# Kernel optimization log

Measured on AMD Instinct MI355X. Metric: run time of the kernel, lower is better.

## Reference

```python
import jax, jax.numpy as jnp
import numpy as np

B, N, C_IN, C_INTER = 32, 2048, 512, 512


def setup_inputs() -> dict:
    key = jax.random.key(0)
    ks = jax.random.split(key, 10)
    s_in = 1.0 / np.sqrt(C_IN)
    s_int = 1.0 / np.sqrt(C_INTER)
    return {
        "query": jax.random.normal(ks[0], (B, N, C_IN), jnp.float32),
        "key": jax.random.normal(ks[1], (B, N, C_IN), jnp.float32),
        "Wq": jax.random.normal(ks[2], (C_IN, C_INTER), jnp.float32) * s_in,
        "bq": jnp.zeros((C_INTER,), jnp.float32),
        "Wk": jax.random.normal(ks[3], (C_IN, C_INTER), jnp.float32) * s_in,
        "bk": jnp.zeros((C_INTER,), jnp.float32),
        "Wv": jax.random.normal(ks[4], (C_IN, C_INTER), jnp.float32) * s_in,
        "bv": jnp.zeros((C_INTER,), jnp.float32),
        "Wo": jax.random.normal(ks[5], (C_INTER, C_INTER), jnp.float32) * s_int,
        "bo": jnp.zeros((C_INTER,), jnp.float32),
    }


def reference(query, key, Wq, bq, Wk, bk, Wv, bv, Wo, bo):
    value = key  # value defaults to key in original forward
    q = jnp.einsum("bnc,cd->bnd", query, Wq) + bq   # [B,N,D]
    k = jnp.einsum("bnc,cd->bnd", key, Wk) + bk
    v = jnp.einsum("bnc,cd->bnd", value, Wv) + bv
    d = q.shape[-1]
    # non-standard scaling: divide by d (not sqrt(d))
    scores = jnp.einsum("bqd,bkd->bqk", q, k) / d    # [B,N,N]
    attn = jax.nn.softmax(scores, axis=-1)
    n_kv = attn.shape[-1]
    # second non-standard scaling: divide by number of keys
    out = jnp.einsum("bqk,bkd->bqd", attn, v) / n_kv
    return jnp.einsum("bnd,de->bne", out, Wo) + bo
```

## Files before the change

### kernel.cpp

```cpp
#include <hip/hip_runtime.h>
#include <stdint.h>

typedef unsigned short u16;
typedef __attribute__((ext_vector_type(8))) short bf16x8;
typedef __attribute__((ext_vector_type(4))) float f32x4;
typedef __attribute__((ext_vector_type(2))) unsigned int u32x2;
typedef __attribute__((ext_vector_type(4))) unsigned int u32x4;

__device__ __forceinline__ float bf2f(u16 u) {
  union { unsigned int i; float f; } v; v.i = ((unsigned int)u) << 16; return v.f;
}
__device__ __forceinline__ u16 f2bf(float f) {
  union { float f; unsigned int i; } v; v.f = f;
  unsigned int x = v.i;
  return (u16)((x + 0x7fffu + ((x >> 16) & 1u)) >> 16);
}

__device__ __forceinline__ void async16(const void* g, void* l) {
  __builtin_amdgcn_global_load_lds(
      (const __attribute__((address_space(1))) void*)g,
      (__attribute__((address_space(3))) void*)l, 16, 0, 0);
}

__global__ __launch_bounds__(256) void cast_f32_to_bf16(
    const float* __restrict__ x, u16* __restrict__ y, long n) {
  long i = ((long)blockIdx.x * blockDim.x + threadIdx.x) * 8;
  long stride = (long)gridDim.x * blockDim.x * 8;
  for (long j = i; j < n; j += stride) {
    float4 a = ((const float4*)(x + j))[0];
    float4 b = ((const float4*)(x + j))[1];
    u32x4 o;
    o.x = (unsigned)f2bf(a.x) | ((unsigned)f2bf(a.y) << 16);
    o.y = (unsigned)f2bf(a.z) | ((unsigned)f2bf(a.w) << 16);
    o.z = (unsigned)f2bf(b.x) | ((unsigned)f2bf(b.y) << 16);
    o.w = (unsigned)f2bf(b.z) | ((unsigned)f2bf(b.w) << 16);
    __builtin_nontemporal_store(o, (u32x4*)(y + j));
  }
}

__global__ __launch_bounds__(256) void castKT(
    const float* __restrict__ Kin, u16* __restrict__ Kb, u16* __restrict__ KbT) {
  __shared__ u16 tile[32][34];
  int t = threadIdx.x;
  long b = blockIdx.z;
  int n0 = blockIdx.x * 32, c0 = blockIdx.y * 32;
  int nr = t >> 3, c4 = (t & 7) * 4;
  float4 v = *(const float4*)(Kin + (b * 2048 + n0 + nr) * 512 + c0 + c4);
  unsigned q0 = f2bf(v.x), q1 = f2bf(v.y), q2 = f2bf(v.z), q3 = f2bf(v.w);
  u32x2 o1; o1.x = q0 | (q1 << 16); o1.y = q2 | (q3 << 16);
  __builtin_nontemporal_store(o1, (u32x2*)(Kb + (b * 2048 + n0 + nr) * 512 + c0 + c4));
  tile[nr][c4] = (u16)q0; tile[nr][c4 + 1] = (u16)q1;
  tile[nr][c4 + 2] = (u16)q2; tile[nr][c4 + 3] = (u16)q3;
  __syncthreads();
  int cr = t >> 3, n4 = (t & 7) * 4;
  unsigned r0 = tile[n4][cr], r1 = tile[n4 + 1][cr];
  unsigned r2 = tile[n4 + 2][cr], r3 = tile[n4 + 3][cr];
  u32x2 o2; o2.x = r0 | (r1 << 16); o2.y = r2 | (r3 << 16);
  __builtin_nontemporal_store(o2, (u32x2*)(KbT + (b * 512 + c0 + cr) * 2048 + n0 + n4));
}

__global__ __launch_bounds__(256) void smallGT(
    const float* __restrict__ Ai, const float* __restrict__ Bi, u16* __restrict__ C) {
  __shared__ float As[16][65], Bs[16][65];
  int t = threadIdx.x;
  int i0 = blockIdx.y * 16, j0 = blockIdx.x * 16;
  int r = t >> 4, c4 = (t & 15) * 4;
  int ty = t >> 4, tx = t & 15;
  float acc = 0.f;
  for (int d0 = 0; d0 < 512; d0 += 64) {
    float4 a = *(const float4*)(Ai + (i0 + r) * 512 + d0 + c4);
    float4 b = *(const float4*)(Bi + (j0 + r) * 512 + d0 + c4);
    __syncthreads();
    As[r][c4] = a.x; As[r][c4 + 1] = a.y; As[r][c4 + 2] = a.z; As[r][c4 + 3] = a.w;
    Bs[r][c4] = b.x; Bs[r][c4 + 1] = b.y; Bs[r][c4 + 2] = b.z; Bs[r][c4 + 3] = b.w;
    __syncthreads();
#pragma unroll
    for (int d = 0; d < 64; ++d) acc += As[ty][d] * Bs[tx][d];
  }
  C[(i0 + ty) * 512 + j0 + tx] = f2bf(acc);
}

__global__ __launch_bounds__(256) void smallW2T(
    const float* __restrict__ Wv, const float* __restrict__ Wo, u16* __restrict__ C) {
  __shared__ float Vs[16][65];
  __shared__ float Os[64][17];
  int t = threadIdx.x;
  int k0 = blockIdx.x * 16, n0 = blockIdx.y * 16;
  int r = t >> 4, c4 = (t & 15) * 4;
  int dd = t >> 2, nn4 = (t & 3) * 4;
  int ty = t >> 4, tx = t & 15;
  float acc = 0.f;
  for (int d0 = 0; d0 < 512; d0 += 64) {
    float4 a = *(const float4*)(Wv + (k0 + r) * 512 + d0 + c4);
    float4 b = *(const float4*)(Wo + (long)(d0 + dd) * 512 + n0 + nn4);
    __syncthreads();
    Vs[r][c4] = a.x; Vs[r][c4 + 1] = a.y; Vs[r][c4 + 2] = a.z; Vs[r][c4 + 3] = a.w;
    Os[dd][nn4] = b.x; Os[dd][nn4 + 1] = b.y; Os[dd][nn4 + 2] = b.z; Os[dd][nn4 + 3] = b.w;
    __syncthreads();
#pragma unroll
    for (int d = 0; d < 64; ++d) acc += Vs[tx][d] * Os[d][ty];
  }
  C[(n0 + ty) * 512 + k0 + tx] = f2bf(acc);
}

__global__ __launch_bounds__(256) void wveck(
    const float* __restrict__ Wk, const float* __restrict__ bq, float* __restrict__ wv) {
  int c = blockIdx.x, t = threadIdx.x;
  float s = 0.f;
  for (int d = t; d < 512; d += 256) s += Wk[c * 512 + d] * bq[d];
  for (int off = 32; off; off >>= 1) s += __shfl_xor(s, off);
  __shared__ float r4[4];
  if ((t & 63) == 0) r4[t >> 6] = s;
  __syncthreads();
  if (t == 0) wv[c] = (r4[0] + r4[1] + r4[2] + r4[3]) * (1.0f / 512.0f);
}

__global__ __launch_bounds__(256) void cveck(
    const float* __restrict__ Wo, const float* __restrict__ bv,
    const float* __restrict__ bo, float* __restrict__ c2) {
  int e = blockIdx.x * 256 + threadIdx.x;
  float s = 0.f;
  for (int d = 0; d < 512; ++d) s += bv[d] * Wo[d * 512 + e];
  c2[e] = s * (1.0f / 2048.0f) + bo[e];
}

__global__ __launch_bounds__(256) void betak(
    const u16* __restrict__ Kb, const float* __restrict__ wv, float* __restrict__ beta) {
  __shared__ float ws[512];
  int t = threadIdx.x, lane = t & 63, wid = t >> 6;
  ws[t] = wv[t];
  ws[t + 256] = wv[t + 256];
  __syncthreads();
  long row = (long)blockIdx.x * 4 + wid;
  bf16x8 v = *(const bf16x8*)(Kb + row * 512 + lane * 8);
  float s = 0.f;
#pragma unroll
  for (int j = 0; j < 8; ++j) s += bf2f((u16)v[j]) * ws[lane * 8 + j];
  for (int off = 32; off; off >>= 1) s += __shfl_xor(s, off);
  if (lane == 0) beta[row] = s;
}

__global__ __launch_bounds__(256) void rowred(
    const float* __restrict__ psum, float* __restrict__ rinv, int nrows) {
  int r = blockIdx.x * 256 + threadIdx.x;
  if (r >= nrows) return;
  const float* p = psum + (long)r * 32;
  float s = 0.f;
#pragma unroll
  for (int j = 0; j < 32; ++j) s += p[j];
  rinv[r] = 1.0f / s;
}

template <int MODE, int EXPO>
__global__ __launch_bounds__(256, 3) void gemm(
    const u16* __restrict__ A, const u16* __restrict__ B,
    const float* __restrict__ bias, long sBias,
    const float* __restrict__ rsc, float* __restrict__ psum,
    void* __restrict__ Cout,
    int N, int K, long sA, long sB, long sC, float scale,
    int mT, int nT, int Z, int nfast) {
  __shared__ __align__(16) char lds[2][24576];
  const int t = threadIdx.x;
  const int lane = t & 63;
  const int w = t >> 6;
  const int wm = w >> 1;
  const int wn = w & 1;

  const int wg = blockIdx.x;
  const int nb = mT * nT;
  long z; int within;
  if (Z > 1 && (Z & 7) == 0) {
    int xcd = wg & 7, sub = wg >> 3;
    z = (long)(sub / nb) * 8 + xcd;
    within = sub % nb;
  } else { z = wg / nb; within = wg % nb; }
  int bx, by;
  if (nfast) { by = within % nT; bx = within / nT; }
  else       { bx = within % mT; by = within / mT; }
  const long m0 = (long)bx * 256;
  const int n0 = by * 128;
  const int nt = K >> 5;

  const int srow = w * 16 + (lane >> 2);
  const int koff = 8 * ((lane & 3) ^ ((lane >> 3) & 3));
  const u16* pa = A + z * sA + (m0 + srow) * (long)K + koff;
  const u16* pb = B + z * sB + ((long)(n0 + srow)) * K + koff;
  const int ldsW = w * 1024;

  const int fr = lane & 15;
  const int kb = (lane >> 4) * 16;
  const int sw = ((fr >> 1) & 3) << 4;
  const int aoff = (wm * 128 + fr) * 64 + (kb ^ sw);
  const int boff = 16384 + (wn * 64 + fr) * 64 + (kb ^ sw);

  f32x4 acc[8][4] = {};

#define STAGE(BUF)                                                         \
  do {                                                                     \
    char* d_ = lds[BUF] + ldsW;                                            \
    _Pragma("unroll") for (int c = 0; c < 4; ++c)                          \
        async16(pa + (long)c * 64 * K, d_ + c * 4096);                     \
    _Pragma("unroll") for (int c = 0; c < 2; ++c)                          \
        async16(pb + (long)c * 64 * K, d_ + 16384 + c * 4096);             \
    pa += 32; pb += 32;                                                    \
  } while (0)

  STAGE(0);
  __syncthreads();

  int cur = 0;
  for (int tt = 0; tt < nt; ++tt) {
    if (tt + 1 < nt) STAGE(cur ^ 1);
    const char* rb = lds[cur];
    bf16x8 bf[4];
#pragma unroll
    for (int ni = 0; ni < 4; ++ni)
      bf[ni] = *(const bf16x8*)(rb + boff + ni * 1024);
    __builtin_amdgcn_s_setprio(1);
#pragma unroll
    for (int mi = 0; mi < 8; ++mi) {
      bf16x8 af = *(const bf16x8*)(rb + aoff + mi * 1024);
#pragma unroll
      for (int ni = 0; ni < 4; ++ni)
        acc[mi][ni] = __builtin_amdgcn_mfma_f32_16x16x32_bf16(af, bf[ni], acc[mi][ni], 0, 0, 0);
    }
    __builtin_amdgcn_s_setprio(0);
    __syncthreads();
    cur ^= 1;
  }
#undef STAGE

  const int er = (lane >> 4) * 4;
  const int ec = lane & 15;
  float bvv[4];
#pragma unroll
  for (int ni = 0; ni < 4; ++ni)
    bvv[ni] = bias ? bias[z * sBias + n0 + wn * 64 + ni * 16 + ec] : 0.0f;
  if (MODE == 0) {
    u16* Ep = (u16*)lds;
    u16* Cp = (u16*)Cout + z * sC;
#pragma unroll
    for (int p = 0; p < 2; ++p) {
      __syncthreads();
      if (wm == p) {
#pragma unroll
        for (int mi = 0; mi < 8; ++mi) {
#pragma unroll
          for (int i = 0; i < 4; ++i) {
            int lrow = mi * 16 + er + i;
            float rv = 1.0f;
            if (!EXPO && rsc) rv = rsc[z * 2048 + m0 + wm * 128 + lrow];
            float rs = 0.f;
#pragma unroll
            for (int ni = 0; ni < 4; ++ni) {
              float val = acc[mi][ni][i] * scale + bvv[ni];
              if (EXPO) { val = __expf(val); rs += val; }
              else val *= rv;
              Ep[lrow * 136 + wn * 64 + ni * 16 + ec] = f2bf(val);
            }
            if (EXPO) {
              rs += __shfl_xor(rs, 1);
              rs += __shfl_xor(rs, 2);
              rs += __shfl_xor(rs, 4);
              rs += __shfl_xor(rs, 8);
              if (ec == 0)
                psum[((long)z * 2048 + m0 + wm * 128 + lrow) * 32 + by * 2 + wn] = rs;
            }
          }
        }
      }
      __syncthreads();
#pragma unroll
      for (int s = 0; s < 8; ++s) {
        int idx = s * 256 + t;
        int R = idx >> 4;
        int j = idx & 15;
        u32x4 d = *(const u32x4*)(Ep + R * 136 + j * 8);
        u32x4* dst = (u32x4*)(Cp + (m0 + p * 128 + R) * (long)N + n0 + j * 8);
        if (EXPO) *dst = d;
        else __builtin_nontemporal_store(d, dst);
      }
    }
  } else {
    float* Ep = (float*)lds;
    float* Cp = (float*)Cout + z * sC;
#pragma unroll
    for (int p = 0; p < 4; ++p) {
      __syncthreads();
      if (wm == (p >> 1)) {
#pragma unroll
        for (int mi2 = 0; mi2 < 4; ++mi2) {
          int mi = (p & 1) * 4 + mi2;
#pragma unroll
          for (int ni = 0; ni < 4; ++ni)
#pragma unroll
            for (int i = 0; i < 4; ++i)
              Ep[(mi2 * 16 + er + i) * 132 + wn * 64 + ni * 16 + ec] =
                  acc[mi][ni][i] * scale + bvv[ni];
        }
      }
      __syncthreads();
#pragma unroll
      for (int s = 0; s < 8; ++s) {
        int idx = s * 256 + t;
        int R = idx >> 5;
        int j = idx & 31;
        f32x4 d = *(const f32x4*)(Ep + R * 132 + j * 4);
        __builtin_nontemporal_store(
            d, (f32x4*)(Cp + (m0 + p * 64 + R) * (long)N + n0 + j * 4));
      }
    }
  }
}

extern "C" void kernel_launch(void* const* d_in, const int* in_sizes, int n_in,
                              void* d_out, int out_size, void* d_ws, size_t ws_size,
                              hipStream_t stream) {
  const float* query = (const float*)d_in[0];
  const float* key_  = (const float*)d_in[1];
  const float* Wq = (const float*)d_in[2];
  const float* bq = (const float*)d_in[3];
  const float* Wk = (const float*)d_in[4];
  const float* bk = (const float*)d_in[5];
  const float* Wv = (const float*)d_in[6];
  const float* bv = (const float*)d_in[7];
  const float* Wo = (const float*)d_in[8];
  const float* bo = (const float*)d_in[9];
  (void)bk;
  float* out = (float*)d_out;

  const long tokE = 65536L * 512;
  const long bstride = 2048L * 512;

  char* ws = (char*)d_ws;
  u16* Qb   = (u16*)(ws);
  u16* Kb   = (u16*)(ws + 67108864L);
  u16* KbT  = (u16*)(ws + 134217728L);
  u16* GT   = (u16*)(ws + 201326592L);
  u16* W2T  = (u16*)(ws + 201850880L);
  float* wv   = (float*)(ws + 202375168L);
  float* c2   = (float*)(ws + 202377216L);
  float* beta = (float*)(ws + 202379264L);
  float* rinv = (float*)(ws + 202641408L);
  char* Sbase = ws + 203423744L;
  u16* attn = Qb;

  u16* qb = (u16*)d_out;
  float* psum = (float*)((char*)d_out + 67108864L);

  long s_avail = (long)ws_size - 203423744L;
  int g = (int)(s_avail / 8388608L);
  if (g < 1) g = 1;
  if (g > 32) g = 32;
  if (g >= 8) g &= ~7;

  cast_f32_to_bf16<<<16384, 256, 0, stream>>>(query, Qb, tokE);
  castKT<<<dim3(64, 16, 32), 256, 0, stream>>>(key_, Kb, KbT);
  smallGT<<<dim3(32, 32), 256, 0, stream>>>(Wk, Wq, GT);
  smallW2T<<<dim3(32, 32), 256, 0, stream>>>(Wv, Wo, W2T);
  wveck<<<512, 256, 0, stream>>>(Wk, bq, wv);
  cveck<<<2, 256, 0, stream>>>(Wo, bv, bo, c2);
  betak<<<16384, 256, 0, stream>>>(Kb, wv, beta);

  gemm<0, 0><<<256 * 4, 256, 0, stream>>>(
      Qb, GT, nullptr, 0, nullptr, nullptr, qb,
      512, 512, 0, 0, 0, 1.0f, 256, 4, 1, 0);

  for (int b0 = 0; b0 < 32; b0 += g) {
    int bc = (32 - b0 < g) ? (32 - b0) : g;
    u16* Sg = (u16*)Sbase;
    gemm<0, 1><<<8 * 16 * bc, 256, 0, stream>>>(
        qb + (long)b0 * bstride, Kb + (long)b0 * bstride,
        beta + (long)b0 * 2048, 2048, nullptr, psum, Sg, 2048, 512,
        bstride, bstride, 2048L * 2048, 1.0f / 512.0f, 8, 16, bc, 0);
    rowred<<<(bc * 2048 + 255) / 256, 256, 0, stream>>>(psum, rinv, bc * 2048);
    gemm<0, 0><<<8 * 4 * bc, 256, 0, stream>>>(
        Sg, KbT + (long)b0 * bstride, nullptr, 0, rinv, nullptr,
        attn + (long)b0 * bstride, 512, 2048,
        2048L * 2048, bstride, bstride, 1.0f / 2048.0f, 8, 4, bc, 1);
  }

  gemm<2, 0><<<256 * 4, 256, 0, stream>>>(
      attn, W2T, c2, 0, nullptr, nullptr, out,
      512, 512, 0, 0, 0, 1.0f, 256, 4, 1, 0);
}
```

Before: 713.0 us.

## Reassociate output projection into value path before attention PV GEMM

Computes K·(Wv·Wo) once per token up front, transposes it, and has the attention-times-value GEMM write fp32 output directly with the bias vector and row softmax normalization applied in its epilogue. This removes the final bf16 attn intermediate and the separate output-projection GEMM. It adds a dense projection GEMM plus a transpose over the keys, and replaces the fused cast+transpose of K with a plain cast. The row-scale support is added to the fp32 epilogue path, and workspace is reshuffled so d_out serves as scratch for Qb and the temporary.

```diff
diff --git a/kernel.cpp b/kernel.cpp
--- a/kernel.cpp
+++ b/kernel.cpp
@@ -38,25 +38,24 @@
   }
 }
 
-__global__ __launch_bounds__(256) void castKT(
-    const float* __restrict__ Kin, u16* __restrict__ Kb, u16* __restrict__ KbT) {
+__global__ __launch_bounds__(256) void transB(
+    const u16* __restrict__ src, u16* __restrict__ dst) {
   __shared__ u16 tile[32][34];
   int t = threadIdx.x;
   long b = blockIdx.z;
   int n0 = blockIdx.x * 32, c0 = blockIdx.y * 32;
   int nr = t >> 3, c4 = (t & 7) * 4;
-  float4 v = *(const float4*)(Kin + (b * 2048 + n0 + nr) * 512 + c0 + c4);
-  unsigned q0 = f2bf(v.x), q1 = f2bf(v.y), q2 = f2bf(v.z), q3 = f2bf(v.w);
-  u32x2 o1; o1.x = q0 | (q1 << 16); o1.y = q2 | (q3 << 16);
-  __builtin_nontemporal_store(o1, (u32x2*)(Kb + (b * 2048 + n0 + nr) * 512 + c0 + c4));
-  tile[nr][c4] = (u16)q0; tile[nr][c4 + 1] = (u16)q1;
-  tile[nr][c4 + 2] = (u16)q2; tile[nr][c4 + 3] = (u16)q3;
+  u32x2 v = *(const u32x2*)(src + (b * 2048 + n0 + nr) * 512 + c0 + c4);
+  tile[nr][c4]     = (u16)(v.x & 0xffffu);
+  tile[nr][c4 + 1] = (u16)(v.x >> 16);
+  tile[nr][c4 + 2] = (u16)(v.y & 0xffffu);
+  tile[nr][c4 + 3] = (u16)(v.y >> 16);
   __syncthreads();
   int cr = t >> 3, n4 = (t & 7) * 4;
   unsigned r0 = tile[n4][cr], r1 = tile[n4 + 1][cr];
   unsigned r2 = tile[n4 + 2][cr], r3 = tile[n4 + 3][cr];
-  u32x2 o2; o2.x = r0 | (r1 << 16); o2.y = r2 | (r3 << 16);
-  __builtin_nontemporal_store(o2, (u32x2*)(KbT + (b * 512 + c0 + cr) * 2048 + n0 + n4));
+  u32x2 o; o.x = r0 | (r1 << 16); o.y = r2 | (r3 << 16);
+  __builtin_nontemporal_store(o, (u32x2*)(dst + (b * 512 + c0 + cr) * 2048 + n0 + n4));
 }
 
 __global__ __launch_bounds__(256) void smallGT(
@@ -276,9 +275,8 @@
         int R = idx >> 4;
         int j = idx & 15;
         u32x4 d = *(const u32x4*)(Ep + R * 136 + j * 8);
-        u32x4* dst = (u32x4*)(Cp + (m0 + p * 128 + R) * (long)N + n0 + j * 8);
-        if (EXPO) *dst = d;
-        else __builtin_nontemporal_store(d, dst);
+        __builtin_nontemporal_store(
+            d, (u32x4*)(Cp + (m0 + p * 128 + R) * (long)N + n0 + j * 8));
       }
     }
   } else {
@@ -292,11 +290,14 @@
         for (int mi2 = 0; mi2 < 4; ++mi2) {
           int mi = (p & 1) * 4 + mi2;
 #pragma unroll
-          for (int ni = 0; ni < 4; ++ni)
-#pragma unroll
-            for (int i = 0; i < 4; ++i)
+          for (int i = 0; i < 4; ++i) {
+            float rv = 1.0f;
+            if (rsc) rv = rsc[z * 2048 + m0 + wm * 128 + mi * 16 + er + i];
+#pragma unroll
+            for (int ni = 0; ni < 4; ++ni)
               Ep[(mi2 * 16 + er + i) * 132 + wn * 64 + ni * 16 + ec] =
-                  acc[mi][ni][i] * scale + bvv[ni];
+                  acc[mi][ni][i] * scale * rv + bvv[ni];
+          }
         }
       }
       __syncthreads();
@@ -333,29 +334,29 @@
   const long bstride = 2048L * 512;
 
   char* ws = (char*)d_ws;
-  u16* Qb   = (u16*)(ws);
-  u16* Kb   = (u16*)(ws + 67108864L);
-  u16* KbT  = (u16*)(ws + 134217728L);
+  u16* Kb   = (u16*)(ws);
+  u16* V2T  = (u16*)(ws + 67108864L);
+  u16* qb   = (u16*)(ws + 134217728L);
   u16* GT   = (u16*)(ws + 201326592L);
   u16* W2T  = (u16*)(ws + 201850880L);
   float* wv   = (float*)(ws + 202375168L);
   float* c2   = (float*)(ws + 202377216L);
   float* beta = (float*)(ws + 202379264L);
   float* rinv = (float*)(ws + 202641408L);
-  char* Sbase = ws + 203423744L;
-  u16* attn = Qb;
-
-  u16* qb = (u16*)d_out;
+  char* Sbase = ws + 202903552L;
+
+  u16* Qb = (u16*)d_out;
+  u16* V2tmp = (u16*)d_out;
   float* psum = (float*)((char*)d_out + 67108864L);
 
-  long s_avail = (long)ws_size - 203423744L;
+  long s_avail = (long)ws_size - 202903552L;
   int g = (int)(s_avail / 8388608L);
   if (g < 1) g = 1;
   if (g > 32) g = 32;
   if (g >= 8) g &= ~7;
 
   cast_f32_to_bf16<<<16384, 256, 0, stream>>>(query, Qb, tokE);
-  castKT<<<dim3(64, 16, 32), 256, 0, stream>>>(key_, Kb, KbT);
+  cast_f32_to_bf16<<<16384, 256, 0, stream>>>(key_, Kb, tokE);
   smallGT<<<dim3(32, 32), 256, 0, stream>>>(Wk, Wq, GT);
   smallW2T<<<dim3(32, 32), 256, 0, stream>>>(Wv, Wo, W2T);
   wveck<<<512, 256, 0, stream>>>(Wk, bq, wv);
@@ -365,6 +366,11 @@
   gemm<0, 0><<<256 * 4, 256, 0, stream>>>(
       Qb, GT, nullptr, 0, nullptr, nullptr, qb,
       512, 512, 0, 0, 0, 1.0f, 256, 4, 1, 0);
+
+  gemm<0, 0><<<256 * 4, 256, 0, stream>>>(
+      Kb, W2T, nullptr, 0, nullptr, nullptr, V2tmp,
+      512, 512, 0, 0, 0, 1.0f, 256, 4, 1, 0);
+  transB<<<dim3(64, 16, 32), 256, 0, stream>>>(V2tmp, V2T);
 
   for (int b0 = 0; b0 < 32; b0 += g) {
     int bc = (32 - b0 < g) ? (32 - b0) : g;
@@ -374,13 +380,9 @@
         beta + (long)b0 * 2048, 2048, nullptr, psum, Sg, 2048, 512,
         bstride, bstride, 2048L * 2048, 1.0f / 512.0f, 8, 16, bc, 0);
     rowred<<<(bc * 2048 + 255) / 256, 256, 0, stream>>>(psum, rinv, bc * 2048);
-    gemm<0, 0><<<8 * 4 * bc, 256, 0, stream>>>(
-        Sg, KbT + (long)b0 * bstride, nullptr, 0, rinv, nullptr,
-        attn + (long)b0 * bstride, 512, 2048,
+    gemm<2, 0><<<8 * 4 * bc, 256, 0, stream>>>(
+        Sg, V2T + (long)b0 * bstride, c2, 0, rinv, nullptr,
+        out + (long)b0 * bstride, 512, 2048,
         2048L * 2048, bstride, bstride, 1.0f / 2048.0f, 8, 4, bc, 1);
   }
-
-  gemm<2, 0><<<256 * 4, 256, 0, stream>>>(
-      attn, W2T, c2, 0, nullptr, nullptr, out,
-      512, 512, 0, 0, 0, 1.0f, 256, 4, 1, 0);
-}
+}
```

Result: faster. 696.2 us (-2.3%).
